# Kernel optimization log

Hardware: AMD Instinct MI355X
Metric: run time of the kernel (lower is better)

Reference implementation:

```python
import jax, jax.numpy as jnp
import numpy as np

N_PROT = 20000   # protein table rows
D = 256          # hidden_dim
T = 262144       # total (drug, pathway, protein) memberships
G = 16384        # number of (drug, pathway) groups
N_DRUGS = 4096


def setup_inputs() -> dict:
    key = jax.random.key(0)
    k1, k2, k3, k4, k5, k6 = jax.random.split(key, 6)
    protein_h = jax.random.normal(k1, (N_PROT, D), dtype=jnp.float32)
    member_protein_idx = jax.random.randint(k2, (T,), 0, N_PROT)
    member_seg = jnp.sort(jax.random.randint(k3, (T,), 0, G))
    group_to_drug = jnp.sort(jax.random.randint(k4, (G,), 0, N_DRUGS))
    attn_w = jax.random.normal(k5, (D,), dtype=jnp.float32) / np.sqrt(D)
    proj_W = jax.random.normal(k6, (D, D), dtype=jnp.float32) / np.sqrt(D)
    proj_b = jnp.zeros((D,), dtype=jnp.float32)
    return dict(protein_h=protein_h, member_protein_idx=member_protein_idx,
                member_seg=member_seg, group_to_drug=group_to_drug,
                attn_w=attn_w, proj_W=proj_W, proj_b=proj_b)


def reference(protein_h, member_protein_idx, member_seg, group_to_drug,
              attn_w, proj_W, proj_b):
    # Gather protein embeddings for all (drug, pathway) memberships.  [T, D]
    ph = protein_h[member_protein_idx]
    # Attention logits (Linear(D, 1, bias=False)).  [T]
    s = ph @ attn_w
    # Segment softmax within each pathway group (stable).
    smax = jax.ops.segment_max(s, member_seg, num_segments=G)
    smax = jax.lax.stop_gradient(jnp.where(jnp.isfinite(smax), smax, 0.0))
    e = jnp.exp(s - smax[member_seg])
    denom = jax.ops.segment_sum(e, member_seg, num_segments=G)
    w = e / denom[member_seg]                                    # [T]
    # Attention-weighted pool per pathway group.  [G, D]
    pooled = jax.ops.segment_sum(w[:, None] * ph, member_seg, num_segments=G)
    # Mean over non-empty pathway groups per drug.
    cnt = jax.ops.segment_sum(jnp.ones_like(s), member_seg, num_segments=G)
    nonempty = (cnt > 0).astype(protein_h.dtype)                 # [G]
    drug_sum = jax.ops.segment_sum(pooled, group_to_drug, num_segments=N_DRUGS)
    drug_cnt = jax.ops.segment_sum(nonempty, group_to_drug, num_segments=N_DRUGS)
    out = drug_sum / jnp.maximum(drug_cnt, 1.0)[:, None]          # [N_DRUGS, D]
    # Dropout is identity at eval time; final projection + ReLU.
    return jax.nn.relu(out @ proj_W.T + proj_b)
```

## Files before the change

### kernel.cpp

```cpp
#include <hip/hip_runtime.h>
#include <math.h>

#define HD 256

typedef unsigned int uint32;
typedef __attribute__((ext_vector_type(8))) short bf16x8;
typedef __attribute__((ext_vector_type(4))) float f32x4;

__device__ inline unsigned short f2bf(float f) {
  uint32 u = __float_as_uint(f);
  return (unsigned short)((u + 0x7fffu + ((u >> 16) & 1u)) >> 16);
}
__device__ inline float bflo(uint32 v) { return __uint_as_float(v << 16); }
__device__ inline float bfhi(uint32 v) { return __uint_as_float(v & 0xffff0000u); }

__global__ __launch_bounds__(256) void prep_kernel(
    const int* __restrict__ mseg, int T, int G, int* __restrict__ gstart,
    const int* __restrict__ g2d, int ND, int* __restrict__ dstart,
    const float* __restrict__ W, int NW, unsigned short* __restrict__ Wbf,
    const float* __restrict__ protein_h, const float* __restrict__ attn_w,
    int np, float* __restrict__ etbl, unsigned short* __restrict__ wph,
    int nbb) {
  int b = blockIdx.x;
  if (b < nbb) {
    int t = b * 256 + threadIdx.x;
    if (t <= T) {
      int cur  = (t < T) ? mseg[t] : G;
      int prev = (t == 0) ? -1 : mseg[t - 1];
      for (int g = prev + 1; g <= cur; ++g) gstart[g] = t;
    }
    if (t <= G) {
      int cur  = (t < G) ? g2d[t] : ND;
      int prev = (t == 0) ? -1 : g2d[t - 1];
      for (int d = prev + 1; d <= cur; ++d) dstart[d] = t;
    }
    if (t < NW) Wbf[t] = f2bf(W[t]);
    return;
  }
  int wave = threadIdx.x >> 6, lane = threadIdx.x & 63;
  int p = (b - nbb) * 4 + wave;
  if (p >= np) return;
  float4 w = ((const float4*)attn_w)[lane];
  float4 v = ((const float4*)(protein_h + (size_t)p * HD))[lane];
  float s = v.x * w.x + v.y * w.y + v.z * w.z + v.w * w.w;
#pragma unroll
  for (int o = 32; o > 0; o >>= 1) s += __shfl_xor(s, o, 64);
  float e = __expf(s);
  if (lane == 0) etbl[p] = e;
  ushort4 st;
  st.x = f2bf(e * v.x); st.y = f2bf(e * v.y);
  st.z = f2bf(e * v.z); st.w = f2bf(e * v.w);
  *(ushort4*)(wph + ((size_t)(lane >> 4) * np + p) * 64 + (lane & 15) * 4) = st;
}

__global__ __launch_bounds__(64) void group_pool_kernel(
    const unsigned short* __restrict__ wph, const int* __restrict__ midx,
    const float* __restrict__ etbl, const int* __restrict__ gstart,
    int G, int np, unsigned short* __restrict__ pooled) {
  int lane = threadIdx.x;
  int B = blockIdx.x;
  int xcd = B & 7;
  int chunk = xcd >> 1;
  int gpair = (B >> 3) * 2 + (xcd & 1);
  int g0 = gpair * 2;
  if (g0 >= G) return;
  const unsigned short* slice = wph + (size_t)chunk * np * 64;
  int quarter = lane >> 4, qlane = lane & 15;
  for (int gi = 0; gi < 2; ++gi) {
    int g = g0 + gi;
    if (g >= G) break;
    int beg = gstart[g], end = gstart[g + 1];
    ushort4 st = make_ushort4(0, 0, 0, 0);
    if (beg < end) {
      float4 acc = make_float4(0.f, 0.f, 0.f, 0.f);
      float denom = 0.f;
      for (int c = beg; c < end; c += 64) {
        int cn = end - c; if (cn > 64) cn = 64;
        int myrow = midx[c + (lane < cn ? lane : 0)];
        if (lane < cn) denom += etbl[myrow];
#pragma unroll 4
        for (int t = 0; t < cn; t += 4) {
          int src = t + quarter;
          int row = __shfl(myrow, src, 64);
          if (src < cn) {
            uint2 v = *(const uint2*)(slice + ((size_t)row << 6) + (qlane << 2));
            acc.x += bflo(v.x); acc.y += bfhi(v.x);
            acc.z += bflo(v.y); acc.w += bfhi(v.y);
          }
        }
      }
#pragma unroll
      for (int o = 32; o > 0; o >>= 1) denom += __shfl_xor(denom, o, 64);
      acc.x += __shfl_xor(acc.x, 16, 64); acc.x += __shfl_xor(acc.x, 32, 64);
      acc.y += __shfl_xor(acc.y, 16, 64); acc.y += __shfl_xor(acc.y, 32, 64);
      acc.z += __shfl_xor(acc.z, 16, 64); acc.z += __shfl_xor(acc.z, 32, 64);
      acc.w += __shfl_xor(acc.w, 16, 64); acc.w += __shfl_xor(acc.w, 32, 64);
      float inv = 1.f / denom;
      st.x = f2bf(acc.x * inv); st.y = f2bf(acc.y * inv);
      st.z = f2bf(acc.z * inv); st.w = f2bf(acc.w * inv);
    }
    if (quarter == 0)
      *(ushort4*)(pooled + ((size_t)g << 8) + (chunk << 6) + (qlane << 2)) = st;
  }
}

#define GM 16
__global__ __launch_bounds__(512) void mean_gemm_kernel(
    const unsigned short* __restrict__ pooled, const int* __restrict__ gstart,
    const int* __restrict__ dstart, const unsigned short* __restrict__ Wbf,
    const float* __restrict__ bias, float* __restrict__ out) {
  __shared__ unsigned short Abf[GM][HD + 8];
  int wave = threadIdx.x >> 6, lane = threadIdx.x & 63;
  int m0 = blockIdx.x * GM;

  for (int dd = 0; dd < 2; ++dd) {
    int d = m0 + wave * 2 + dd;
    int beg = dstart[d], end = dstart[d + 1];
    float4 acc = make_float4(0.f, 0.f, 0.f, 0.f);
    float cnt = 0.f;
    for (int g = beg; g < end; ++g) {
      if (gstart[g + 1] > gstart[g]) {
        uint2 v = *(const uint2*)(pooled + ((size_t)g << 8) + (lane << 2));
        acc.x += bflo(v.x); acc.y += bfhi(v.x);
        acc.z += bflo(v.y); acc.w += bfhi(v.y);
        cnt += 1.f;
      }
    }
    float inv = 1.f / fmaxf(cnt, 1.f);
    ushort4 st;
    st.x = f2bf(acc.x * inv); st.y = f2bf(acc.y * inv);
    st.z = f2bf(acc.z * inv); st.w = f2bf(acc.w * inv);
    *(ushort4*)&Abf[wave * 2 + dd][lane * 4] = st;
  }
  __syncthreads();

  int n0 = wave * 32;
  int arow = lane & 15;
  int apack = lane >> 4;
  f32x4 acc[2] = {};
#pragma unroll
  for (int k0 = 0; k0 < HD; k0 += 32) {
    int k = k0 + apack * 8;
    bf16x8 af = *(const bf16x8*)&Abf[arow][k];
#pragma unroll
    for (int t = 0; t < 2; ++t) {
      int col = n0 + t * 16 + arow;
      bf16x8 bfr = *(const bf16x8*)(Wbf + (size_t)col * HD + k);
      acc[t] = __builtin_amdgcn_mfma_f32_16x16x32_bf16(af, bfr, acc[t], 0, 0, 0);
    }
  }
  int rbase = m0 + (lane >> 4) * 4;
#pragma unroll
  for (int t = 0; t < 2; ++t) {
    int col = n0 + t * 16 + (lane & 15);
    float bv = bias[col];
#pragma unroll
    for (int j = 0; j < 4; ++j) {
      out[(size_t)(rbase + j) * HD + col] = fmaxf(acc[t][j] + bv, 0.f);
    }
  }
}

extern "C" void kernel_launch(void* const* d_in, const int* in_sizes, int n_in,
                              void* d_out, int out_size, void* d_ws, size_t ws_size,
                              hipStream_t stream) {
  const float* protein_h = (const float*)d_in[0];
  const int*   midx      = (const int*)d_in[1];
  const int*   mseg      = (const int*)d_in[2];
  const int*   g2d       = (const int*)d_in[3];
  const float* attn_w    = (const float*)d_in[4];
  const float* proj_W    = (const float*)d_in[5];
  const float* proj_b    = (const float*)d_in[6];
  float* out = (float*)d_out;

  const int NPROT = in_sizes[0] / HD;
  const int T  = in_sizes[1];
  const int G  = in_sizes[3];
  const int NW = in_sizes[5];
  const int ND = out_size / HD;

  char* ws = (char*)d_ws;
  int* gstart = (int*)ws;
  int* dstart = gstart + (G + 1);
  size_t off = (((size_t)(G + 1) + (size_t)(ND + 1)) * sizeof(int) + 255) & ~(size_t)255;
  float* etbl = (float*)(ws + off);
  off += (((size_t)NPROT * sizeof(float)) + 255) & ~(size_t)255;
  unsigned short* Wbf = (unsigned short*)(ws + off);
  off += (((size_t)NW * sizeof(unsigned short)) + 255) & ~(size_t)255;
  unsigned short* wph = (unsigned short*)(ws + off);
  off += (((size_t)NPROT * HD * sizeof(unsigned short)) + 255) & ~(size_t)255;
  unsigned short* pooled = (unsigned short*)(ws + off);

  int nmax = (T > G ? T : G) + 1;
  int nbb = (nmax + 255) / 256;
  int npb = (NPROT + 3) / 4;
  prep_kernel<<<nbb + npb, 256, 0, stream>>>(
      mseg, T, G, gstart, g2d, ND, dstart, proj_W, NW, Wbf,
      protein_h, attn_w, NPROT, etbl, wph, nbb);
  int gpairs = (G + 1) / 2;
  int nblk = 8 * ((gpairs + 1) / 2);
  group_pool_kernel<<<nblk, 64, 0, stream>>>(
      wph, midx, etbl, gstart, G, NPROT, pooled);
  mean_gemm_kernel<<<ND / GM, 512, 0, stream>>>(
      pooled, gstart, dstart, Wbf, proj_b, out);
}
```

Before: 55.15 us.

## Precompute per-member softmax coefficients and pool directly per drug

A new coef_kernel computes each group's softmax denominator and writes a (protein row, 1/denom) pair for every membership. The pooling kernel then works per drug instead of per group: it walks all memberships of the drug's groups and accumulates coefficient-weighted embeddings straight into a drug mean. The intermediate pooled [G, D] buffer is gone, and the GEMM kernel reads the drug means directly with no shared-memory averaging stage. In exchange there is an extra kernel launch and an 8-byte-per-member coefficient buffer to write and read, and work per block now varies with drug size, so load balance may be worse.

```diff
diff --git a/kernel.cpp b/kernel.cpp
--- a/kernel.cpp
+++ b/kernel.cpp
@@ -53,87 +53,82 @@
   *(ushort4*)(wph + ((size_t)(lane >> 4) * np + p) * 64 + (lane & 15) * 4) = st;
 }
 
-__global__ __launch_bounds__(64) void group_pool_kernel(
-    const unsigned short* __restrict__ wph, const int* __restrict__ midx,
-    const float* __restrict__ etbl, const int* __restrict__ gstart,
-    int G, int np, unsigned short* __restrict__ pooled) {
+__global__ __launch_bounds__(256) void coef_kernel(
+    const int* __restrict__ midx, const float* __restrict__ etbl,
+    const int* __restrict__ gstart, int G, uint2* __restrict__ cw) {
+  int q = blockIdx.x * 16 + (threadIdx.x >> 4);
+  int ql = threadIdx.x & 15;
+  if (q >= G) return;
+  int beg = gstart[q], end = gstart[q + 1];
+  if (beg >= end) return;
+  float d = 0.f;
+  for (int c = beg + ql; c < end; c += 16) d += etbl[midx[c]];
+  d += __shfl_xor(d, 1, 64); d += __shfl_xor(d, 2, 64);
+  d += __shfl_xor(d, 4, 64); d += __shfl_xor(d, 8, 64);
+  float inv = 1.f / d;
+  for (int c = beg + ql; c < end; c += 16) {
+    cw[c] = make_uint2((uint32)midx[c], __float_as_uint(inv));
+  }
+}
+
+__global__ __launch_bounds__(64) void drug_pool_kernel(
+    const unsigned short* __restrict__ wph, const uint2* __restrict__ cw,
+    const int* __restrict__ gstart, const int* __restrict__ dstart,
+    int ND, int np, unsigned short* __restrict__ dmean) {
   int lane = threadIdx.x;
   int B = blockIdx.x;
   int xcd = B & 7;
   int chunk = xcd >> 1;
-  int gpair = (B >> 3) * 2 + (xcd & 1);
-  int g0 = gpair * 2;
-  if (g0 >= G) return;
+  int d0 = ((B >> 3) * 2 + (xcd & 1)) * 2;
+  if (d0 >= ND) return;
   const unsigned short* slice = wph + (size_t)chunk * np * 64;
   int quarter = lane >> 4, qlane = lane & 15;
-  for (int gi = 0; gi < 2; ++gi) {
-    int g = g0 + gi;
-    if (g >= G) break;
-    int beg = gstart[g], end = gstart[g + 1];
-    ushort4 st = make_ushort4(0, 0, 0, 0);
-    if (beg < end) {
-      float4 acc = make_float4(0.f, 0.f, 0.f, 0.f);
-      float denom = 0.f;
-      for (int c = beg; c < end; c += 64) {
-        int cn = end - c; if (cn > 64) cn = 64;
-        int myrow = midx[c + (lane < cn ? lane : 0)];
-        if (lane < cn) denom += etbl[myrow];
+  for (int di = 0; di < 2; ++di) {
+    int d = d0 + di;
+    if (d >= ND) break;
+    int gb = dstart[d], ge = dstart[d + 1];
+    int mbeg = gstart[gb], mend = gstart[ge];
+    int cnt = 0;
+    for (int base = gb; base < ge; base += 64) {
+      int gg = base + lane;
+      bool ne = (gg < ge) && (gstart[gg + 1] > gstart[gg]);
+      cnt += (int)__popcll(__ballot(ne));
+    }
+    float4 acc = make_float4(0.f, 0.f, 0.f, 0.f);
+    for (int c = mbeg; c < mend; c += 64) {
+      int cn = mend - c; if (cn > 64) cn = 64;
 #pragma unroll 4
-        for (int t = 0; t < cn; t += 4) {
-          int src = t + quarter;
-          int row = __shfl(myrow, src, 64);
-          if (src < cn) {
-            uint2 v = *(const uint2*)(slice + ((size_t)row << 6) + (qlane << 2));
-            acc.x += bflo(v.x); acc.y += bfhi(v.x);
-            acc.z += bflo(v.y); acc.w += bfhi(v.y);
-          }
+      for (int t = 0; t < cn; t += 4) {
+        int src = t + quarter;
+        if (src < cn) {
+          uint2 cwv = cw[c + src];
+          float cf = __uint_as_float(cwv.y);
+          uint2 v = *(const uint2*)(slice + ((size_t)cwv.x << 6) + (qlane << 2));
+          acc.x += cf * bflo(v.x); acc.y += cf * bfhi(v.x);
+          acc.z += cf * bflo(v.y); acc.w += cf * bfhi(v.y);
         }
       }
-#pragma unroll
-      for (int o = 32; o > 0; o >>= 1) denom += __shfl_xor(denom, o, 64);
-      acc.x += __shfl_xor(acc.x, 16, 64); acc.x += __shfl_xor(acc.x, 32, 64);
-      acc.y += __shfl_xor(acc.y, 16, 64); acc.y += __shfl_xor(acc.y, 32, 64);
-      acc.z += __shfl_xor(acc.z, 16, 64); acc.z += __shfl_xor(acc.z, 32, 64);
-      acc.w += __shfl_xor(acc.w, 16, 64); acc.w += __shfl_xor(acc.w, 32, 64);
-      float inv = 1.f / denom;
+    }
+    acc.x += __shfl_xor(acc.x, 16, 64); acc.x += __shfl_xor(acc.x, 32, 64);
+    acc.y += __shfl_xor(acc.y, 16, 64); acc.y += __shfl_xor(acc.y, 32, 64);
+    acc.z += __shfl_xor(acc.z, 16, 64); acc.z += __shfl_xor(acc.z, 32, 64);
+    acc.w += __shfl_xor(acc.w, 16, 64); acc.w += __shfl_xor(acc.w, 32, 64);
+    float inv = 1.f / fmaxf((float)cnt, 1.f);
+    if (quarter == 0) {
+      ushort4 st;
       st.x = f2bf(acc.x * inv); st.y = f2bf(acc.y * inv);
       st.z = f2bf(acc.z * inv); st.w = f2bf(acc.w * inv);
-    }
-    if (quarter == 0)
-      *(ushort4*)(pooled + ((size_t)g << 8) + (chunk << 6) + (qlane << 2)) = st;
+      *(ushort4*)(dmean + (size_t)d * HD + (chunk << 6) + (qlane << 2)) = st;
+    }
   }
 }
 
 #define GM 16
-__global__ __launch_bounds__(512) void mean_gemm_kernel(
-    const unsigned short* __restrict__ pooled, const int* __restrict__ gstart,
-    const int* __restrict__ dstart, const unsigned short* __restrict__ Wbf,
+__global__ __launch_bounds__(512) void gemm_kernel(
+    const unsigned short* __restrict__ A, const unsigned short* __restrict__ Wbf,
     const float* __restrict__ bias, float* __restrict__ out) {
-  __shared__ unsigned short Abf[GM][HD + 8];
   int wave = threadIdx.x >> 6, lane = threadIdx.x & 63;
   int m0 = blockIdx.x * GM;
-
-  for (int dd = 0; dd < 2; ++dd) {
-    int d = m0 + wave * 2 + dd;
-    int beg = dstart[d], end = dstart[d + 1];
-    float4 acc = make_float4(0.f, 0.f, 0.f, 0.f);
-    float cnt = 0.f;
-    for (int g = beg; g < end; ++g) {
-      if (gstart[g + 1] > gstart[g]) {
-        uint2 v = *(const uint2*)(pooled + ((size_t)g << 8) + (lane << 2));
-        acc.x += bflo(v.x); acc.y += bfhi(v.x);
-        acc.z += bflo(v.y); acc.w += bfhi(v.y);
-        cnt += 1.f;
-      }
-    }
-    float inv = 1.f / fmaxf(cnt, 1.f);
-    ushort4 st;
-    st.x = f2bf(acc.x * inv); st.y = f2bf(acc.y * inv);
-    st.z = f2bf(acc.z * inv); st.w = f2bf(acc.w * inv);
-    *(ushort4*)&Abf[wave * 2 + dd][lane * 4] = st;
-  }
-  __syncthreads();
-
   int n0 = wave * 32;
   int arow = lane & 15;
   int apack = lane >> 4;
@@ -141,7 +136,7 @@
 #pragma unroll
   for (int k0 = 0; k0 < HD; k0 += 32) {
     int k = k0 + apack * 8;
-    bf16x8 af = *(const bf16x8*)&Abf[arow][k];
+    bf16x8 af = *(const bf16x8*)(A + (size_t)(m0 + arow) * HD + k);
 #pragma unroll
     for (int t = 0; t < 2; ++t) {
       int col = n0 + t * 16 + arow;
@@ -189,7 +184,9 @@
   off += (((size_t)NW * sizeof(unsigned short)) + 255) & ~(size_t)255;
   unsigned short* wph = (unsigned short*)(ws + off);
   off += (((size_t)NPROT * HD * sizeof(unsigned short)) + 255) & ~(size_t)255;
-  unsigned short* pooled = (unsigned short*)(ws + off);
+  uint2* cw = (uint2*)(ws + off);
+  off += (((size_t)T * sizeof(uint2)) + 255) & ~(size_t)255;
+  unsigned short* dmean = (unsigned short*)(ws + off);
 
   int nmax = (T > G ? T : G) + 1;
   int nbb = (nmax + 255) / 256;
@@ -197,10 +194,8 @@
   prep_kernel<<<nbb + npb, 256, 0, stream>>>(
       mseg, T, G, gstart, g2d, ND, dstart, proj_W, NW, Wbf,
       protein_h, attn_w, NPROT, etbl, wph, nbb);
-  int gpairs = (G + 1) / 2;
-  int nblk = 8 * ((gpairs + 1) / 2);
-  group_pool_kernel<<<nblk, 64, 0, stream>>>(
-      wph, midx, etbl, gstart, G, NPROT, pooled);
-  mean_gemm_kernel<<<ND / GM, 512, 0, stream>>>(
-      pooled, gstart, dstart, Wbf, proj_b, out);
-}
+  coef_kernel<<<(G + 15) / 16, 256, 0, stream>>>(midx, etbl, gstart, G, cw);
+  drug_pool_kernel<<<8 * ((ND + 3) / 4), 64, 0, stream>>>(
+      wph, cw, gstart, dstart, ND, NPROT, dmean);
+  gemm_kernel<<<ND / GM, 512, 0, stream>>>(dmean, Wbf, proj_b, out);
+}
```

Result: slower. 60.45 us (+9.6%).
